# Optimization experiments

Measured on AMD Instinct MI355X. Metric: run time of the kernel, lower is better.

## Reference

```python
import jax, jax.numpy as jnp
import numpy as np

B, S, H = 2, 2048, 2048
NH, HD = 32, 64          # num heads, head dim (H = NH*HD)
ROT = 16                 # rotary_ndims = int(HD * rope_pct=0.25)
THETA = 10000.0
MAXPOS = 4096
NEG_INF = -1e30


def _rope_cache():
    inv_freq = 1.0 / (THETA ** (jnp.arange(0, ROT, 2, dtype=jnp.float32) / ROT))
    t = jnp.arange(MAXPOS, dtype=jnp.float32)
    freqs = jnp.outer(t, inv_freq)              # [MAXPOS, ROT/2]
    emb = jnp.concatenate([freqs, freqs], -1)   # [MAXPOS, ROT]
    return jnp.cos(emb), jnp.sin(emb)


def _rotate_half(x):
    x1, x2 = jnp.split(x, 2, axis=-1)
    return jnp.concatenate([-x2, x1], axis=-1)


def setup_inputs() -> dict:
    key = jax.random.key(0)
    k1, k2, k3 = jax.random.split(key, 3)
    hidden_states = jax.random.normal(k1, (B, S, H), dtype=jnp.float32)
    qkv_w = jax.random.normal(k2, (3 * H, H), dtype=jnp.float32) * 0.02
    o_w = jax.random.normal(k3, (H, H), dtype=jnp.float32) * 0.02
    position_ids = (jnp.arange(B * S).reshape(B, S) % MAXPOS).astype(jnp.int32)
    return {"hidden_states": hidden_states, "qkv_w": qkv_w, "o_w": o_w,
            "position_ids": position_ids}


def reference(hidden_states, qkv_w, o_w, position_ids):
    b, s, _ = hidden_states.shape
    # fused QKV projection (Linear, no bias): x @ W^T
    qkv = hidden_states @ qkv_w.T                      # [b, s, 3H]
    q, k, v = jnp.split(qkv, 3, axis=-1)
    # (b, s, nh*hd) -> (b, nh, s, hd)
    q = q.reshape(b, s, NH, HD).transpose(0, 2, 1, 3)
    k = k.reshape(b, s, NH, HD).transpose(0, 2, 1, 3)
    v = v.reshape(b, s, NH, HD).transpose(0, 2, 1, 3)

    # partial RoPE on first ROT dims
    cos, sin = _rope_cache()
    cos = cos[position_ids][:, None]                   # [b, 1, s, ROT]
    sin = sin[position_ids][:, None]
    q_rot, q_pass = q[..., :ROT], q[..., ROT:]
    k_rot, k_pass = k[..., :ROT], k[..., ROT:]
    q_rot = q_rot * cos + _rotate_half(q_rot) * sin
    k_rot = k_rot * cos + _rotate_half(k_rot) * sin
    q = jnp.concatenate([q_rot, q_pass], axis=-1)
    k = jnp.concatenate([k_rot, k_pass], axis=-1)

    # causal scaled-dot-product attention (prefill branch, layer_past=None)
    scale = 1.0 / jnp.sqrt(jnp.float32(HD))
    scores = jnp.einsum('bhqd,bhkd->bhqk', q, k) * scale
    causal = jnp.tril(jnp.ones((s, s), dtype=bool))
    scores = jnp.where(causal, scores, NEG_INF)
    weights = jax.nn.softmax(scores.astype(jnp.float32), axis=-1).astype(q.dtype)
    attn = jnp.einsum('bhqk,bhkd->bhqd', weights, v)   # [b, nh, s, hd]

    attn = attn.transpose(0, 2, 1, 3).reshape(b, s, NH * HD)
    return attn @ o_w.T
```

## Files before the change

kernel.cpp:

```cpp
#include <hip/hip_runtime.h>
#include <hip/hip_bf16.h>
#include <math.h>

#define B_   2
#define S_   2048
#define H_   2048
#define NH_  32
#define HD_  64

typedef __bf16 bf16_t;
typedef bf16_t bf16x8 __attribute__((ext_vector_type(8)));
typedef float  f32x4  __attribute__((ext_vector_type(4)));

__device__ __forceinline__ float bf2f(unsigned short u) {
  unsigned int x = ((unsigned int)u) << 16;
  return __builtin_bit_cast(float, x);
}
__device__ __forceinline__ unsigned short f2bf(float f) {
  unsigned int u = __builtin_bit_cast(unsigned int, f);
  u += 0x7FFFu + ((u >> 16) & 1u);
  return (unsigned short)(u >> 16);
}

__device__ __forceinline__ void gload16(const void* g, void* l) {
  __builtin_amdgcn_global_load_lds((const __attribute__((address_space(1))) void*)g,
                                   (__attribute__((address_space(3))) void*)l, 16, 0, 0);
}

__global__ void cast_kernel(const float* __restrict__ in, unsigned short* __restrict__ out, int n4) {
  int stride = gridDim.x * blockDim.x;
  for (int i = blockIdx.x * blockDim.x + threadIdx.x; i < n4; i += stride) {
    float4 v = reinterpret_cast<const float4*>(in)[i];
    ushort4 o;
    o.x = f2bf(v.x); o.y = f2bf(v.y); o.z = f2bf(v.z); o.w = f2bf(v.w);
    reinterpret_cast<ushort4*>(out)[i] = o;
  }
}

template<int EPI>
__global__ __launch_bounds__(256) void gemm_bt(
    const unsigned short* __restrict__ A, const unsigned short* __restrict__ Bt,
    float* __restrict__ outF,
    unsigned short* __restrict__ qb, unsigned short* __restrict__ kb, unsigned short* __restrict__ vt,
    int M, int N, int K)
{
  __shared__ unsigned short As[128 * 64];
  __shared__ unsigned short Bs[128 * 64];
  const int tid  = threadIdx.x;
  const int lane = tid & 63;
  const int wave = tid >> 6;
  const int lo = lane & 15, hi = lane >> 4;
  const int wr = wave >> 1, wc = wave & 1;
  const int m0 = blockIdx.x * 128;
  const int n0 = blockIdx.y * 128;

  const unsigned short* asrc[4];
  const unsigned short* bsrc[4];
  unsigned short* adst[4];
  unsigned short* bdst[4];
#pragma unroll
  for (int i = 0; i < 4; ++i) {
    int idx = i * 256 + tid;
    int r  = idx >> 3;
    int cb = (idx & 7) * 16;
    int cs = cb ^ ((r & 7) << 4);
    asrc[i] = A  + (size_t)(m0 + r) * K + (cs >> 1);
    bsrc[i] = Bt + (size_t)(n0 + r) * K + (cs >> 1);
    adst[i] = &As[idx * 8];
    bdst[i] = &Bs[idx * 8];
  }

  f32x4 zero = {0.f, 0.f, 0.f, 0.f};
  f32x4 acc[4][4];
#pragma unroll
  for (int i = 0; i < 4; ++i)
#pragma unroll
    for (int j = 0; j < 4; ++j) acc[i][j] = zero;

  for (int k0 = 0; k0 < K; k0 += 64) {
    __syncthreads();
#pragma unroll
    for (int i = 0; i < 4; ++i) gload16(asrc[i] + k0, adst[i]);
#pragma unroll
    for (int i = 0; i < 4; ++i) gload16(bsrc[i] + k0, bdst[i]);
    __syncthreads();
#pragma unroll
    for (int kk = 0; kk < 2; ++kk) {
      bf16x8 af[4], bfm[4];
#pragma unroll
      for (int i = 0; i < 4; ++i) {
        int ra = wr * 64 + i * 16 + lo;
        af[i] = *reinterpret_cast<const bf16x8*>(
            (const char*)As + ra * 128 + ((kk * 64 + hi * 16) ^ ((ra & 7) << 4)));
        int rb = wc * 64 + i * 16 + lo;
        bfm[i] = *reinterpret_cast<const bf16x8*>(
            (const char*)Bs + rb * 128 + ((kk * 64 + hi * 16) ^ ((rb & 7) << 4)));
      }
#pragma unroll
      for (int i = 0; i < 4; ++i)
#pragma unroll
        for (int j = 0; j < 4; ++j)
          acc[i][j] = __builtin_amdgcn_mfma_f32_16x16x32_bf16(af[i], bfm[j], acc[i][j], 0, 0, 0);
    }
  }

#pragma unroll
  for (int i = 0; i < 4; ++i) {
#pragma unroll
    for (int j = 0; j < 4; ++j) {
#pragma unroll
      for (int r = 0; r < 4; ++r) {
        int row = m0 + wr * 64 + i * 16 + hi * 4 + r;
        int col = n0 + wc * 64 + j * 16 + lo;
        float v = acc[i][j][r];
        if (EPI == 0) {
          int sec = col >> 11;
          int hh  = (col >> 6) & 31;
          int d   = col & 63;
          int b   = row >> 11;
          int s   = row & 2047;
          unsigned short bv = f2bf(v);
          if (sec == 0)      qb[((size_t)(b * NH_ + hh) * S_ + s) * HD_ + d] = bv;
          else if (sec == 1) kb[((size_t)(b * NH_ + hh) * S_ + s) * HD_ + d] = bv;
          else               vt[((size_t)(b * NH_ + hh) * HD_ + d) * S_ + s] = bv;
        } else {
          outF[(size_t)row * N + col] = v;
        }
      }
    }
  }
}

__global__ void rope_kernel(unsigned short* __restrict__ qb, unsigned short* __restrict__ kb,
                            const int* __restrict__ pos) {
  int idx = blockIdx.x * blockDim.x + threadIdx.x;
  if (idx >= B_ * NH_ * S_) return;
  int s  = idx & (S_ - 1);
  int bh = idx >> 11;
  int b  = bh >> 5;
  float p = (float)pos[b * S_ + s];
  const float invf[8] = {1.0f, 0.31622776601683794f, 0.1f, 0.031622776601683791f,
                         0.01f, 0.0031622776601683794f, 0.001f, 0.00031622776601683794f};
  unsigned short* q = qb + (size_t)idx * HD_;
  unsigned short* k = kb + (size_t)idx * HD_;
#pragma unroll
  for (int i = 0; i < 8; ++i) {
    float ang = p * invf[i];
    float sn, c;
    sincosf(ang, &sn, &c);
    float q1 = bf2f(q[i]), q2 = bf2f(q[i + 8]);
    q[i]     = f2bf(q1 * c - q2 * sn);
    q[i + 8] = f2bf(q2 * c + q1 * sn);
    float k1 = bf2f(k[i]), k2 = bf2f(k[i + 8]);
    k[i]     = f2bf(k1 * c - k2 * sn);
    k[i + 8] = f2bf(k2 * c + k1 * sn);
  }
}

__global__ __launch_bounds__(256) void attn_fwd(
    const unsigned short* __restrict__ qb, const unsigned short* __restrict__ kb,
    const unsigned short* __restrict__ vt, unsigned short* __restrict__ ob)
{
  __shared__ unsigned short Ks[2][64 * 64];
  __shared__ unsigned short Vs[2][64 * 64];
  __shared__ unsigned short Ps[4][32 * 64];
  const int qt   = (int)gridDim.x - 1 - (int)blockIdx.x;
  const int bh   = blockIdx.y;
  const int tid  = threadIdx.x;
  const int lane = tid & 63;
  const int wave = tid >> 6;
  const int lo = lane & 15, hi = lane >> 4;
  const int b = bh >> 5, h = bh & 31;
  const unsigned short* Qg = qb + (size_t)bh * S_ * HD_;
  const unsigned short* Kg = kb + (size_t)bh * S_ * HD_;
  const unsigned short* Vg = vt + (size_t)bh * HD_ * S_;

  bf16x8 aq[2][2];
#pragma unroll
  for (int rf = 0; rf < 2; ++rf)
#pragma unroll
    for (int kk = 0; kk < 2; ++kk) {
      bf16x8 t = *reinterpret_cast<const bf16x8*>(
          Qg + (size_t)(qt * 128 + wave * 32 + rf * 16 + lo) * HD_ + kk * 32 + hi * 8);
#pragma unroll
      for (int e = 0; e < 8; ++e) aq[rf][kk][e] = (bf16_t)((float)t[e] * 0.125f);
    }

  f32x4 zero = {0.f, 0.f, 0.f, 0.f};
  float m_s[2][4], l_s[2][4];
  f32x4 o_acc[2][4];
#pragma unroll
  for (int rf = 0; rf < 2; ++rf)
#pragma unroll
    for (int r = 0; r < 4; ++r) { m_s[rf][r] = -1e30f; l_s[rf][r] = 0.f; }
#pragma unroll
  for (int rf = 0; rf < 2; ++rf)
#pragma unroll
    for (int dt = 0; dt < 4; ++dt) o_acc[rf][dt] = zero;

  auto stage = [&](int kt, int buf) {
#pragma unroll
    for (int i = 0; i < 2; ++i) {
      int idx = i * 256 + tid;
      int r   = idx >> 3;
      int cs  = ((idx & 7) * 16) ^ ((r & 7) << 4);
      gload16(Kg + (size_t)(kt * 64 + r) * HD_ + (cs >> 1), &Ks[buf][idx * 8]);
      gload16(Vg + (size_t)r * S_ + kt * 64 + (cs >> 1), &Vs[buf][idx * 8]);
    }
  };

  const int nkt = 2 * qt + 2;
  stage(0, 0);

  for (int kt = 0; kt < nkt; ++kt) {
    const int cur = kt & 1;
    if (kt + 1 < nkt) {
      stage(kt + 1, cur ^ 1);
      asm volatile("s_waitcnt vmcnt(4)" ::: "memory");
    } else {
      asm volatile("s_waitcnt vmcnt(0)" ::: "memory");
    }
    __builtin_amdgcn_s_barrier();
    __builtin_amdgcn_sched_barrier(0);

    bf16x8 bk[4][2];
#pragma unroll
    for (int ct = 0; ct < 4; ++ct)
#pragma unroll
      for (int kk = 0; kk < 2; ++kk) {
        int row = ct * 16 + lo;
        bk[ct][kk] = *reinterpret_cast<const bf16x8*>(
            (const char*)&Ks[cur][0] + row * 128 + ((kk * 64 + hi * 16) ^ ((row & 7) << 4)));
      }
    f32x4 sc[2][4];
    __builtin_amdgcn_s_setprio(1);
#pragma unroll
    for (int rf = 0; rf < 2; ++rf)
#pragma unroll
      for (int ct = 0; ct < 4; ++ct) {
        f32x4 a = zero;
        a = __builtin_amdgcn_mfma_f32_16x16x32_bf16(aq[rf][0], bk[ct][0], a, 0, 0, 0);
        a = __builtin_amdgcn_mfma_f32_16x16x32_bf16(aq[rf][1], bk[ct][1], a, 0, 0, 0);
        sc[rf][ct] = a;
      }
    __builtin_amdgcn_s_setprio(0);

    if (kt >= nkt - 2) {
#pragma unroll
      for (int rf = 0; rf < 2; ++rf)
#pragma unroll
        for (int ct = 0; ct < 4; ++ct)
#pragma unroll
          for (int rr = 0; rr < 4; ++rr) {
            int qrow = qt * 128 + wave * 32 + rf * 16 + hi * 4 + rr;
            int kcol = kt * 64 + ct * 16 + lo;
            if (kcol > qrow) sc[rf][ct][rr] = -1e30f;
          }
    }

#pragma unroll
    for (int rf = 0; rf < 2; ++rf) {
#pragma unroll
      for (int rr = 0; rr < 4; ++rr) {
        float tm = fmaxf(fmaxf(sc[rf][0][rr], sc[rf][1][rr]),
                         fmaxf(sc[rf][2][rr], sc[rf][3][rr]));
        tm = fmaxf(tm, __shfl_xor(tm, 1));
        tm = fmaxf(tm, __shfl_xor(tm, 2));
        tm = fmaxf(tm, __shfl_xor(tm, 4));
        tm = fmaxf(tm, __shfl_xor(tm, 8));
        float mn = fmaxf(m_s[rf][rr], tm);
        float corr = __expf(m_s[rf][rr] - mn);
        m_s[rf][rr] = mn;
        float rs = 0.f;
#pragma unroll
        for (int ct = 0; ct < 4; ++ct) {
          float e = __expf(sc[rf][ct][rr] - mn);
          sc[rf][ct][rr] = e;
          rs += e;
        }
        rs += __shfl_xor(rs, 1);
        rs += __shfl_xor(rs, 2);
        rs += __shfl_xor(rs, 4);
        rs += __shfl_xor(rs, 8);
        l_s[rf][rr] = l_s[rf][rr] * corr + rs;
#pragma unroll
        for (int dt = 0; dt < 4; ++dt) o_acc[rf][dt][rr] *= corr;
      }
    }

    char* pw = (char*)&Ps[wave][0];
#pragma unroll
    for (int rf = 0; rf < 2; ++rf)
#pragma unroll
      for (int ct = 0; ct < 4; ++ct)
#pragma unroll
        for (int rr = 0; rr < 4; ++rr) {
          int row = rf * 16 + hi * 4 + rr;
          *(unsigned short*)(pw + row * 128 + ((2 * (ct * 16 + lo)) ^ ((row & 7) << 4))) =
              f2bf(sc[rf][ct][rr]);
        }
    bf16x8 ap[2][2];
#pragma unroll
    for (int rf = 0; rf < 2; ++rf)
#pragma unroll
      for (int kk = 0; kk < 2; ++kk) {
        int rowA = rf * 16 + lo;
        ap[rf][kk] = *reinterpret_cast<const bf16x8*>(
            pw + rowA * 128 + ((kk * 64 + hi * 16) ^ ((rowA & 7) << 4)));
      }

    bf16x8 bv[4][2];
#pragma unroll
    for (int dt = 0; dt < 4; ++dt)
#pragma unroll
      for (int kk = 0; kk < 2; ++kk) {
        int row = dt * 16 + lo;
        bv[dt][kk] = *reinterpret_cast<const bf16x8*>(
            (const char*)&Vs[cur][0] + row * 128 + ((kk * 64 + hi * 16) ^ ((row & 7) << 4)));
      }
    __builtin_amdgcn_s_setprio(1);
#pragma unroll
    for (int rf = 0; rf < 2; ++rf)
#pragma unroll
      for (int dt = 0; dt < 4; ++dt) {
        o_acc[rf][dt] = __builtin_amdgcn_mfma_f32_16x16x32_bf16(ap[rf][0], bv[dt][0], o_acc[rf][dt], 0, 0, 0);
        o_acc[rf][dt] = __builtin_amdgcn_mfma_f32_16x16x32_bf16(ap[rf][1], bv[dt][1], o_acc[rf][dt], 0, 0, 0);
      }
    __builtin_amdgcn_s_setprio(0);

    __builtin_amdgcn_s_barrier();
    __builtin_amdgcn_sched_barrier(0);
  }

#pragma unroll
  for (int rf = 0; rf < 2; ++rf) {
    float inv_l[4];
#pragma unroll
    for (int rr = 0; rr < 4; ++rr) inv_l[rr] = 1.f / l_s[rf][rr];
#pragma unroll
    for (int dt = 0; dt < 4; ++dt)
#pragma unroll
      for (int rr = 0; rr < 4; ++rr) {
        int srow = qt * 128 + wave * 32 + rf * 16 + hi * 4 + rr;
        int d    = dt * 16 + lo;
        ob[(size_t)(b * S_ + srow) * H_ + h * HD_ + d] = f2bf(o_acc[rf][dt][rr] * inv_l[rr]);
      }
  }
}

extern "C" void kernel_launch(void* const* d_in, const int* in_sizes, int n_in,
                              void* d_out, int out_size, void* d_ws, size_t ws_size,
                              hipStream_t stream) {
  (void)in_sizes; (void)n_in; (void)out_size; (void)ws_size;
  const float* hs   = (const float*)d_in[0];
  const float* qkvw = (const float*)d_in[1];
  const float* ow   = (const float*)d_in[2];
  const int*   pos  = (const int*)d_in[3];

  char* ws = (char*)d_ws;
  unsigned short* Xb = (unsigned short*)(ws);
  unsigned short* Wq = (unsigned short*)(ws + (16ull << 20));
  unsigned short* Ob = (unsigned short*)(ws + (40ull << 20));
  unsigned short* Qb = (unsigned short*)(ws + (48ull << 20));
  unsigned short* Kb = (unsigned short*)(ws + (64ull << 20));
  unsigned short* Vt = (unsigned short*)(ws + (80ull << 20));

  cast_kernel<<<2048, 256, 0, stream>>>(hs,   Xb, (B_ * S_ * H_) / 4);
  cast_kernel<<<2048, 256, 0, stream>>>(qkvw, Wq, (3 * H_ * H_) / 4);
  cast_kernel<<<2048, 256, 0, stream>>>(ow,   Ob, (H_ * H_) / 4);

  gemm_bt<0><<<dim3(32, 48), 256, 0, stream>>>(Xb, Wq, nullptr, Qb, Kb, Vt,
                                               B_ * S_, 3 * H_, H_);
  rope_kernel<<<(B_ * NH_ * S_) / 256, 256, 0, stream>>>(Qb, Kb, pos);
  attn_fwd<<<dim3(S_ / 128, B_ * NH_), 256, 0, stream>>>(Qb, Kb, Vt, Xb);
  gemm_bt<1><<<dim3(32, 16), 256, 0, stream>>>(Xb, Ob, (float*)d_out,
                                               nullptr, nullptr, nullptr,
                                               B_ * S_, H_, H_);
}
```

Measured before the change: 572.8 us.

## Widen attention blocks to 256 query rows with triple-buffered KV and causal skip

The attention kernel now uses 512-thread blocks covering 256 query rows, so each staged K/V tile is shared by twice as many waves. K/V staging moves to a 3-deep ring buffer that prefetches two tiles ahead. Waves skip compute on tiles lying wholly above their causal diagonal, and the softmax uses exp2 with log2e folded into the Q scale. In exchange, work per block becomes less balanced across waves, LDS use grows, and the launch-bounds hint may restrict registers.

```diff
diff --git a/kernel.cpp b/kernel.cpp
--- a/kernel.cpp
+++ b/kernel.cpp
@@ -157,13 +157,13 @@
   }
 }
 
-__global__ __launch_bounds__(256) void attn_fwd(
+__global__ __launch_bounds__(512, 3) void attn_fwd(
     const unsigned short* __restrict__ qb, const unsigned short* __restrict__ kb,
     const unsigned short* __restrict__ vt, unsigned short* __restrict__ ob)
 {
-  __shared__ unsigned short Ks[2][64 * 64];
-  __shared__ unsigned short Vs[2][64 * 64];
-  __shared__ unsigned short Ps[4][32 * 64];
+  __shared__ unsigned short Ks[3][64 * 64];
+  __shared__ unsigned short Vs[3][64 * 64];
+  __shared__ unsigned short Ps[8][32 * 64];
   const int qt   = (int)gridDim.x - 1 - (int)blockIdx.x;
   const int bh   = blockIdx.y;
   const int tid  = threadIdx.x;
@@ -175,15 +175,18 @@
   const unsigned short* Kg = kb + (size_t)bh * S_ * HD_;
   const unsigned short* Vg = vt + (size_t)bh * HD_ * S_;
 
+  const int qrow0 = qt * 256 + wave * 32;
+
+  const float qscale = 0.125f * 1.4426950408889634f;
   bf16x8 aq[2][2];
 #pragma unroll
   for (int rf = 0; rf < 2; ++rf)
 #pragma unroll
     for (int kk = 0; kk < 2; ++kk) {
       bf16x8 t = *reinterpret_cast<const bf16x8*>(
-          Qg + (size_t)(qt * 128 + wave * 32 + rf * 16 + lo) * HD_ + kk * 32 + hi * 8);
-#pragma unroll
-      for (int e = 0; e < 8; ++e) aq[rf][kk][e] = (bf16_t)((float)t[e] * 0.125f);
+          Qg + (size_t)(qrow0 + rf * 16 + lo) * HD_ + kk * 32 + hi * 8);
+#pragma unroll
+      for (int e = 0; e < 8; ++e) aq[rf][kk][e] = (bf16_t)((float)t[e] * qscale);
     }
 
   f32x4 zero = {0.f, 0.f, 0.f, 0.f};
@@ -199,134 +202,135 @@
     for (int dt = 0; dt < 4; ++dt) o_acc[rf][dt] = zero;
 
   auto stage = [&](int kt, int buf) {
-#pragma unroll
-    for (int i = 0; i < 2; ++i) {
-      int idx = i * 256 + tid;
-      int r   = idx >> 3;
-      int cs  = ((idx & 7) * 16) ^ ((r & 7) << 4);
-      gload16(Kg + (size_t)(kt * 64 + r) * HD_ + (cs >> 1), &Ks[buf][idx * 8]);
-      gload16(Vg + (size_t)r * S_ + kt * 64 + (cs >> 1), &Vs[buf][idx * 8]);
-    }
+    int r  = tid >> 3;
+    int cs = ((tid & 7) * 16) ^ ((r & 7) << 4);
+    gload16(Kg + (size_t)(kt * 64 + r) * HD_ + (cs >> 1), &Ks[buf][tid * 8]);
+    gload16(Vg + (size_t)r * S_ + kt * 64 + (cs >> 1), &Vs[buf][tid * 8]);
   };
 
-  const int nkt = 2 * qt + 2;
+  const int nkt = 4 * qt + 4;
   stage(0, 0);
+  stage(1, 1);
 
   for (int kt = 0; kt < nkt; ++kt) {
-    const int cur = kt & 1;
-    if (kt + 1 < nkt) {
-      stage(kt + 1, cur ^ 1);
+    const int cur = kt % 3;
+    if (kt + 2 < nkt) {
+      stage(kt + 2, (kt + 2) % 3);
       asm volatile("s_waitcnt vmcnt(4)" ::: "memory");
+    } else if (kt + 2 == nkt) {
+      asm volatile("s_waitcnt vmcnt(2)" ::: "memory");
     } else {
       asm volatile("s_waitcnt vmcnt(0)" ::: "memory");
     }
     __builtin_amdgcn_s_barrier();
     __builtin_amdgcn_sched_barrier(0);
 
-    bf16x8 bk[4][2];
-#pragma unroll
-    for (int ct = 0; ct < 4; ++ct)
-#pragma unroll
-      for (int kk = 0; kk < 2; ++kk) {
-        int row = ct * 16 + lo;
-        bk[ct][kk] = *reinterpret_cast<const bf16x8*>(
-            (const char*)&Ks[cur][0] + row * 128 + ((kk * 64 + hi * 16) ^ ((row & 7) << 4)));
-      }
-    f32x4 sc[2][4];
-    __builtin_amdgcn_s_setprio(1);
-#pragma unroll
-    for (int rf = 0; rf < 2; ++rf)
-#pragma unroll
-      for (int ct = 0; ct < 4; ++ct) {
-        f32x4 a = zero;
-        a = __builtin_amdgcn_mfma_f32_16x16x32_bf16(aq[rf][0], bk[ct][0], a, 0, 0, 0);
-        a = __builtin_amdgcn_mfma_f32_16x16x32_bf16(aq[rf][1], bk[ct][1], a, 0, 0, 0);
-        sc[rf][ct] = a;
-      }
-    __builtin_amdgcn_s_setprio(0);
-
-    if (kt >= nkt - 2) {
+    if (kt * 64 <= qrow0 + 31) {
+      bf16x8 bk[4][2];
+#pragma unroll
+      for (int ct = 0; ct < 4; ++ct)
+#pragma unroll
+        for (int kk = 0; kk < 2; ++kk) {
+          int row = ct * 16 + lo;
+          bk[ct][kk] = *reinterpret_cast<const bf16x8*>(
+              (const char*)&Ks[cur][0] + row * 128 + ((kk * 64 + hi * 16) ^ ((row & 7) << 4)));
+        }
+      f32x4 sc[2][4];
+      __builtin_amdgcn_s_setprio(1);
 #pragma unroll
       for (int rf = 0; rf < 2; ++rf)
 #pragma unroll
+        for (int ct = 0; ct < 4; ++ct) {
+          f32x4 a = zero;
+          a = __builtin_amdgcn_mfma_f32_16x16x32_bf16(aq[rf][0], bk[ct][0], a, 0, 0, 0);
+          a = __builtin_amdgcn_mfma_f32_16x16x32_bf16(aq[rf][1], bk[ct][1], a, 0, 0, 0);
+          sc[rf][ct] = a;
+        }
+      __builtin_amdgcn_s_setprio(0);
+
+      if (kt * 64 + 63 > qrow0) {
+#pragma unroll
+        for (int rf = 0; rf < 2; ++rf)
+#pragma unroll
+          for (int ct = 0; ct < 4; ++ct)
+#pragma unroll
+            for (int rr = 0; rr < 4; ++rr) {
+              int qrow = qrow0 + rf * 16 + hi * 4 + rr;
+              int kcol = kt * 64 + ct * 16 + lo;
+              if (kcol > qrow) sc[rf][ct][rr] = -1e30f;
+            }
+      }
+
+#pragma unroll
+      for (int rf = 0; rf < 2; ++rf) {
+#pragma unroll
+        for (int rr = 0; rr < 4; ++rr) {
+          float tm = fmaxf(fmaxf(sc[rf][0][rr], sc[rf][1][rr]),
+                           fmaxf(sc[rf][2][rr], sc[rf][3][rr]));
+          tm = fmaxf(tm, __shfl_xor(tm, 1));
+          tm = fmaxf(tm, __shfl_xor(tm, 2));
+          tm = fmaxf(tm, __shfl_xor(tm, 4));
+          tm = fmaxf(tm, __shfl_xor(tm, 8));
+          float mn = fmaxf(m_s[rf][rr], tm);
+          float corr = exp2f(m_s[rf][rr] - mn);
+          m_s[rf][rr] = mn;
+          float rs = 0.f;
+#pragma unroll
+          for (int ct = 0; ct < 4; ++ct) {
+            float e = exp2f(sc[rf][ct][rr] - mn);
+            sc[rf][ct][rr] = e;
+            rs += e;
+          }
+          rs += __shfl_xor(rs, 1);
+          rs += __shfl_xor(rs, 2);
+          rs += __shfl_xor(rs, 4);
+          rs += __shfl_xor(rs, 8);
+          l_s[rf][rr] = l_s[rf][rr] * corr + rs;
+#pragma unroll
+          for (int dt = 0; dt < 4; ++dt) o_acc[rf][dt][rr] *= corr;
+        }
+      }
+
+      char* pw = (char*)&Ps[wave][0];
+#pragma unroll
+      for (int rf = 0; rf < 2; ++rf)
+#pragma unroll
         for (int ct = 0; ct < 4; ++ct)
 #pragma unroll
           for (int rr = 0; rr < 4; ++rr) {
-            int qrow = qt * 128 + wave * 32 + rf * 16 + hi * 4 + rr;
-            int kcol = kt * 64 + ct * 16 + lo;
-            if (kcol > qrow) sc[rf][ct][rr] = -1e30f;
+            int row = rf * 16 + hi * 4 + rr;
+            *(unsigned short*)(pw + row * 128 + ((2 * (ct * 16 + lo)) ^ ((row & 7) << 4))) =
+                f2bf(sc[rf][ct][rr]);
           }
-    }
-
-#pragma unroll
-    for (int rf = 0; rf < 2; ++rf) {
-#pragma unroll
-      for (int rr = 0; rr < 4; ++rr) {
-        float tm = fmaxf(fmaxf(sc[rf][0][rr], sc[rf][1][rr]),
-                         fmaxf(sc[rf][2][rr], sc[rf][3][rr]));
-        tm = fmaxf(tm, __shfl_xor(tm, 1));
-        tm = fmaxf(tm, __shfl_xor(tm, 2));
-        tm = fmaxf(tm, __shfl_xor(tm, 4));
-        tm = fmaxf(tm, __shfl_xor(tm, 8));
-        float mn = fmaxf(m_s[rf][rr], tm);
-        float corr = __expf(m_s[rf][rr] - mn);
-        m_s[rf][rr] = mn;
-        float rs = 0.f;
-#pragma unroll
-        for (int ct = 0; ct < 4; ++ct) {
-          float e = __expf(sc[rf][ct][rr] - mn);
-          sc[rf][ct][rr] = e;
-          rs += e;
-        }
-        rs += __shfl_xor(rs, 1);
-        rs += __shfl_xor(rs, 2);
-        rs += __shfl_xor(rs, 4);
-        rs += __shfl_xor(rs, 8);
-        l_s[rf][rr] = l_s[rf][rr] * corr + rs;
-#pragma unroll
-        for (int dt = 0; dt < 4; ++dt) o_acc[rf][dt][rr] *= corr;
-      }
-    }
-
-    char* pw = (char*)&Ps[wave][0];
-#pragma unroll
-    for (int rf = 0; rf < 2; ++rf)
-#pragma unroll
-      for (int ct = 0; ct < 4; ++ct)
-#pragma unroll
-        for (int rr = 0; rr < 4; ++rr) {
-          int row = rf * 16 + hi * 4 + rr;
-          *(unsigned short*)(pw + row * 128 + ((2 * (ct * 16 + lo)) ^ ((row & 7) << 4))) =
-              f2bf(sc[rf][ct][rr]);
-        }
-    bf16x8 ap[2][2];
-#pragma unroll
-    for (int rf = 0; rf < 2; ++rf)
-#pragma unroll
-      for (int kk = 0; kk < 2; ++kk) {
-        int rowA = rf * 16 + lo;
-        ap[rf][kk] = *reinterpret_cast<const bf16x8*>(
-            pw + rowA * 128 + ((kk * 64 + hi * 16) ^ ((rowA & 7) << 4)));
-      }
-
-    bf16x8 bv[4][2];
-#pragma unroll
-    for (int dt = 0; dt < 4; ++dt)
-#pragma unroll
-      for (int kk = 0; kk < 2; ++kk) {
-        int row = dt * 16 + lo;
-        bv[dt][kk] = *reinterpret_cast<const bf16x8*>(
-            (const char*)&Vs[cur][0] + row * 128 + ((kk * 64 + hi * 16) ^ ((row & 7) << 4)));
-      }
-    __builtin_amdgcn_s_setprio(1);
-#pragma unroll
-    for (int rf = 0; rf < 2; ++rf)
-#pragma unroll
-      for (int dt = 0; dt < 4; ++dt) {
-        o_acc[rf][dt] = __builtin_amdgcn_mfma_f32_16x16x32_bf16(ap[rf][0], bv[dt][0], o_acc[rf][dt], 0, 0, 0);
-        o_acc[rf][dt] = __builtin_amdgcn_mfma_f32_16x16x32_bf16(ap[rf][1], bv[dt][1], o_acc[rf][dt], 0, 0, 0);
-      }
-    __builtin_amdgcn_s_setprio(0);
+      bf16x8 ap[2][2];
+#pragma unroll
+      for (int rf = 0; rf < 2; ++rf)
+#pragma unroll
+        for (int kk = 0; kk < 2; ++kk) {
+          int rowA = rf * 16 + lo;
+          ap[rf][kk] = *reinterpret_cast<const bf16x8*>(
+              pw + rowA * 128 + ((kk * 64 + hi * 16) ^ ((rowA & 7) << 4)));
+        }
+
+      bf16x8 bv[4][2];
+#pragma unroll
+      for (int dt = 0; dt < 4; ++dt)
+#pragma unroll
+        for (int kk = 0; kk < 2; ++kk) {
+          int row = dt * 16 + lo;
+          bv[dt][kk] = *reinterpret_cast<const bf16x8*>(
+              (const char*)&Vs[cur][0] + row * 128 + ((kk * 64 + hi * 16) ^ ((row & 7) << 4)));
+        }
+      __builtin_amdgcn_s_setprio(1);
+#pragma unroll
+      for (int rf = 0; rf < 2; ++rf)
+#pragma unroll
+        for (int dt = 0; dt < 4; ++dt) {
+          o_acc[rf][dt] = __builtin_amdgcn_mfma_f32_16x16x32_bf16(ap[rf][0], bv[dt][0], o_acc[rf][dt], 0, 0, 0);
+          o_acc[rf][dt] = __builtin_amdgcn_mfma_f32_16x16x32_bf16(ap[rf][1], bv[dt][1], o_acc[rf][dt], 0, 0, 0);
+        }
+      __builtin_amdgcn_s_setprio(0);
+    }
 
     __builtin_amdgcn_s_barrier();
     __builtin_amdgcn_sched_barrier(0);
@@ -341,7 +345,7 @@
     for (int dt = 0; dt < 4; ++dt)
 #pragma unroll
       for (int rr = 0; rr < 4; ++rr) {
-        int srow = qt * 128 + wave * 32 + rf * 16 + hi * 4 + rr;
+        int srow = qrow0 + rf * 16 + hi * 4 + rr;
         int d    = dt * 16 + lo;
         ob[(size_t)(b * S_ + srow) * H_ + h * HD_ + d] = f2bf(o_acc[rf][dt][rr] * inv_l[rr]);
       }
@@ -372,7 +376,7 @@
   gemm_bt<0><<<dim3(32, 48), 256, 0, stream>>>(Xb, Wq, nullptr, Qb, Kb, Vt,
                                                B_ * S_, 3 * H_, H_);
   rope_kernel<<<(B_ * NH_ * S_) / 256, 256, 0, stream>>>(Qb, Kb, pos);
-  attn_fwd<<<dim3(S_ / 128, B_ * NH_), 256, 0, stream>>>(Qb, Kb, Vt, Xb);
+  attn_fwd<<<dim3(S_ / 256, B_ * NH_), 512, 0, stream>>>(Qb, Kb, Vt, Xb);
   gemm_bt<1><<<dim3(32, 16), 256, 0, stream>>>(Xb, Ob, (float*)d_out,
                                                nullptr, nullptr, nullptr,
                                                B_ * S_, H_, H_);
```

New measurement: 597.2 us. 4.3% more time.

## Pair causal query tiles per block to balance attention work and share K/V loads

Applied to the files above, without the earlier changes.

Each attention block now processes two query tiles, j and 15-j, so every block does the same amount of causal work, and the K/V tiles it stages are shared by both. The grid drops from 1024 to 512 blocks with a flat index, and launch bounds now request two blocks per CU. The softmax switches to exp2f with log2(e) folded into the Q scale. The cost is doubled accumulator and register state per wave and a larger P scratch buffer in LDS, which may limit occupancy.

```diff
diff --git a/kernel.cpp b/kernel.cpp
--- a/kernel.cpp
+++ b/kernel.cpp
@@ -157,15 +157,16 @@
   }
 }
 
-__global__ __launch_bounds__(256) void attn_fwd(
+__global__ __launch_bounds__(256, 2) void attn_fwd(
     const unsigned short* __restrict__ qb, const unsigned short* __restrict__ kb,
     const unsigned short* __restrict__ vt, unsigned short* __restrict__ ob)
 {
   __shared__ unsigned short Ks[2][64 * 64];
   __shared__ unsigned short Vs[2][64 * 64];
-  __shared__ unsigned short Ps[4][32 * 64];
-  const int qt   = (int)gridDim.x - 1 - (int)blockIdx.x;
-  const int bh   = blockIdx.y;
+  __shared__ unsigned short Ps[4][2][32 * 64];
+  const int bid  = blockIdx.x;
+  const int j    = bid >> 6;
+  const int bh   = bid & 63;
   const int tid  = threadIdx.x;
   const int lane = tid & 63;
   const int wave = tid >> 6;
@@ -175,28 +176,35 @@
   const unsigned short* Kg = kb + (size_t)bh * S_ * HD_;
   const unsigned short* Vg = vt + (size_t)bh * HD_ * S_;
 
-  bf16x8 aq[2][2];
-#pragma unroll
-  for (int rf = 0; rf < 2; ++rf)
-#pragma unroll
-    for (int kk = 0; kk < 2; ++kk) {
-      bf16x8 t = *reinterpret_cast<const bf16x8*>(
-          Qg + (size_t)(qt * 128 + wave * 32 + rf * 16 + lo) * HD_ + kk * 32 + hi * 8);
-#pragma unroll
-      for (int e = 0; e < 8; ++e) aq[rf][kk][e] = (bf16_t)((float)t[e] * 0.125f);
-    }
+  const int qt[2]    = {j, 15 - j};
+  const int qrow0[2] = {j * 128 + wave * 32, (15 - j) * 128 + wave * 32};
+
+  const float qscale = 0.125f * 1.4426950408889634f;
+  bf16x8 aq[2][2][2];
+#pragma unroll
+  for (int t = 0; t < 2; ++t)
+#pragma unroll
+    for (int rf = 0; rf < 2; ++rf)
+#pragma unroll
+      for (int kk = 0; kk < 2; ++kk) {
+        bf16x8 tt = *reinterpret_cast<const bf16x8*>(
+            Qg + (size_t)(qrow0[t] + rf * 16 + lo) * HD_ + kk * 32 + hi * 8);
+#pragma unroll
+        for (int e = 0; e < 8; ++e) aq[t][rf][kk][e] = (bf16_t)((float)tt[e] * qscale);
+      }
 
   f32x4 zero = {0.f, 0.f, 0.f, 0.f};
-  float m_s[2][4], l_s[2][4];
-  f32x4 o_acc[2][4];
-#pragma unroll
-  for (int rf = 0; rf < 2; ++rf)
-#pragma unroll
-    for (int r = 0; r < 4; ++r) { m_s[rf][r] = -1e30f; l_s[rf][r] = 0.f; }
-#pragma unroll
-  for (int rf = 0; rf < 2; ++rf)
-#pragma unroll
-    for (int dt = 0; dt < 4; ++dt) o_acc[rf][dt] = zero;
+  float m_s[2][2][4], l_s[2][2][4];
+  f32x4 o_acc[2][2][4];
+#pragma unroll
+  for (int t = 0; t < 2; ++t)
+#pragma unroll
+    for (int rf = 0; rf < 2; ++rf)
+#pragma unroll
+      for (int r = 0; r < 4; ++r) {
+        m_s[t][rf][r] = -1e30f; l_s[t][rf][r] = 0.f;
+        o_acc[t][rf][r] = zero;
+      }
 
   auto stage = [&](int kt, int buf) {
 #pragma unroll
@@ -209,7 +217,7 @@
     }
   };
 
-  const int nkt = 2 * qt + 2;
+  const int nkt = 2 * (15 - j) + 2;
   stage(0, 0);
 
   for (int kt = 0; kt < nkt; ++kt) {
@@ -232,82 +240,79 @@
         bk[ct][kk] = *reinterpret_cast<const bf16x8*>(
             (const char*)&Ks[cur][0] + row * 128 + ((kk * 64 + hi * 16) ^ ((row & 7) << 4)));
       }
-    f32x4 sc[2][4];
-    __builtin_amdgcn_s_setprio(1);
-#pragma unroll
-    for (int rf = 0; rf < 2; ++rf)
-#pragma unroll
-      for (int ct = 0; ct < 4; ++ct) {
-        f32x4 a = zero;
-        a = __builtin_amdgcn_mfma_f32_16x16x32_bf16(aq[rf][0], bk[ct][0], a, 0, 0, 0);
-        a = __builtin_amdgcn_mfma_f32_16x16x32_bf16(aq[rf][1], bk[ct][1], a, 0, 0, 0);
-        sc[rf][ct] = a;
-      }
-    __builtin_amdgcn_s_setprio(0);
-
-    if (kt >= nkt - 2) {
-#pragma unroll
-      for (int rf = 0; rf < 2; ++rf)
-#pragma unroll
-        for (int ct = 0; ct < 4; ++ct)
+
+#pragma unroll
+    for (int t = 0; t < 2; ++t) {
+      if (kt * 64 <= qrow0[t] + 31) {
+        f32x4 sc[2][4];
+        __builtin_amdgcn_s_setprio(1);
+#pragma unroll
+        for (int rf = 0; rf < 2; ++rf)
+#pragma unroll
+          for (int ct = 0; ct < 4; ++ct) {
+            f32x4 a = zero;
+            a = __builtin_amdgcn_mfma_f32_16x16x32_bf16(aq[t][rf][0], bk[ct][0], a, 0, 0, 0);
+            a = __builtin_amdgcn_mfma_f32_16x16x32_bf16(aq[t][rf][1], bk[ct][1], a, 0, 0, 0);
+            sc[rf][ct] = a;
+          }
+        __builtin_amdgcn_s_setprio(0);
+
+        if (kt * 64 + 63 > qrow0[t]) {
+#pragma unroll
+          for (int rf = 0; rf < 2; ++rf)
+#pragma unroll
+            for (int ct = 0; ct < 4; ++ct)
+#pragma unroll
+              for (int rr = 0; rr < 4; ++rr) {
+                int qrow = qrow0[t] + rf * 16 + hi * 4 + rr;
+                int kcol = kt * 64 + ct * 16 + lo;
+                if (kcol > qrow) sc[rf][ct][rr] = -1e30f;
+              }
+        }
+
+#pragma unroll
+        for (int rf = 0; rf < 2; ++rf) {
 #pragma unroll
           for (int rr = 0; rr < 4; ++rr) {
-            int qrow = qt * 128 + wave * 32 + rf * 16 + hi * 4 + rr;
-            int kcol = kt * 64 + ct * 16 + lo;
-            if (kcol > qrow) sc[rf][ct][rr] = -1e30f;
+            float tm = fmaxf(fmaxf(sc[rf][0][rr], sc[rf][1][rr]),
+                             fmaxf(sc[rf][2][rr], sc[rf][3][rr]));
+            tm = fmaxf(tm, __shfl_xor(tm, 1));
+            tm = fmaxf(tm, __shfl_xor(tm, 2));
+            tm = fmaxf(tm, __shfl_xor(tm, 4));
+            tm = fmaxf(tm, __shfl_xor(tm, 8));
+            float mn = fmaxf(m_s[t][rf][rr], tm);
+            float corr = exp2f(m_s[t][rf][rr] - mn);
+            m_s[t][rf][rr] = mn;
+            float rs = 0.f;
+#pragma unroll
+            for (int ct = 0; ct < 4; ++ct) {
+              float e = exp2f(sc[rf][ct][rr] - mn);
+              sc[rf][ct][rr] = e;
+              rs += e;
+            }
+            rs += __shfl_xor(rs, 1);
+            rs += __shfl_xor(rs, 2);
+            rs += __shfl_xor(rs, 4);
+            rs += __shfl_xor(rs, 8);
+            l_s[t][rf][rr] = l_s[t][rf][rr] * corr + rs;
+#pragma unroll
+            for (int dt = 0; dt < 4; ++dt) o_acc[t][rf][dt][rr] *= corr;
           }
-    }
-
-#pragma unroll
-    for (int rf = 0; rf < 2; ++rf) {
-#pragma unroll
-      for (int rr = 0; rr < 4; ++rr) {
-        float tm = fmaxf(fmaxf(sc[rf][0][rr], sc[rf][1][rr]),
-                         fmaxf(sc[rf][2][rr], sc[rf][3][rr]));
-        tm = fmaxf(tm, __shfl_xor(tm, 1));
-        tm = fmaxf(tm, __shfl_xor(tm, 2));
-        tm = fmaxf(tm, __shfl_xor(tm, 4));
-        tm = fmaxf(tm, __shfl_xor(tm, 8));
-        float mn = fmaxf(m_s[rf][rr], tm);
-        float corr = __expf(m_s[rf][rr] - mn);
-        m_s[rf][rr] = mn;
-        float rs = 0.f;
-#pragma unroll
-        for (int ct = 0; ct < 4; ++ct) {
-          float e = __expf(sc[rf][ct][rr] - mn);
-          sc[rf][ct][rr] = e;
-          rs += e;
         }
-        rs += __shfl_xor(rs, 1);
-        rs += __shfl_xor(rs, 2);
-        rs += __shfl_xor(rs, 4);
-        rs += __shfl_xor(rs, 8);
-        l_s[rf][rr] = l_s[rf][rr] * corr + rs;
-#pragma unroll
-        for (int dt = 0; dt < 4; ++dt) o_acc[rf][dt][rr] *= corr;
-      }
-    }
-
-    char* pw = (char*)&Ps[wave][0];
-#pragma unroll
-    for (int rf = 0; rf < 2; ++rf)
-#pragma unroll
-      for (int ct = 0; ct < 4; ++ct)
-#pragma unroll
-        for (int rr = 0; rr < 4; ++rr) {
-          int row = rf * 16 + hi * 4 + rr;
-          *(unsigned short*)(pw + row * 128 + ((2 * (ct * 16 + lo)) ^ ((row & 7) << 4))) =
-              f2bf(sc[rf][ct][rr]);
-        }
-    bf16x8 ap[2][2];
-#pragma unroll
-    for (int rf = 0; rf < 2; ++rf)
-#pragma unroll
-      for (int kk = 0; kk < 2; ++kk) {
-        int rowA = rf * 16 + lo;
-        ap[rf][kk] = *reinterpret_cast<const bf16x8*>(
-            pw + rowA * 128 + ((kk * 64 + hi * 16) ^ ((rowA & 7) << 4)));
-      }
+
+        char* pw = (char*)&Ps[wave][t][0];
+#pragma unroll
+        for (int rf = 0; rf < 2; ++rf)
+#pragma unroll
+          for (int ct = 0; ct < 4; ++ct)
+#pragma unroll
+            for (int rr = 0; rr < 4; ++rr) {
+              int row = rf * 16 + hi * 4 + rr;
+              *(unsigned short*)(pw + row * 128 + ((2 * (ct * 16 + lo)) ^ ((row & 7) << 4))) =
+                  f2bf(sc[rf][ct][rr]);
+            }
+      }
+    }
 
     bf16x8 bv[4][2];
 #pragma unroll
@@ -318,34 +323,51 @@
         bv[dt][kk] = *reinterpret_cast<const bf16x8*>(
             (const char*)&Vs[cur][0] + row * 128 + ((kk * 64 + hi * 16) ^ ((row & 7) << 4)));
       }
-    __builtin_amdgcn_s_setprio(1);
-#pragma unroll
-    for (int rf = 0; rf < 2; ++rf)
-#pragma unroll
-      for (int dt = 0; dt < 4; ++dt) {
-        o_acc[rf][dt] = __builtin_amdgcn_mfma_f32_16x16x32_bf16(ap[rf][0], bv[dt][0], o_acc[rf][dt], 0, 0, 0);
-        o_acc[rf][dt] = __builtin_amdgcn_mfma_f32_16x16x32_bf16(ap[rf][1], bv[dt][1], o_acc[rf][dt], 0, 0, 0);
-      }
-    __builtin_amdgcn_s_setprio(0);
+#pragma unroll
+    for (int t = 0; t < 2; ++t) {
+      if (kt * 64 <= qrow0[t] + 31) {
+        char* pw = (char*)&Ps[wave][t][0];
+        bf16x8 ap[2][2];
+#pragma unroll
+        for (int rf = 0; rf < 2; ++rf)
+#pragma unroll
+          for (int kk = 0; kk < 2; ++kk) {
+            int rowA = rf * 16 + lo;
+            ap[rf][kk] = *reinterpret_cast<const bf16x8*>(
+                pw + rowA * 128 + ((kk * 64 + hi * 16) ^ ((rowA & 7) << 4)));
+          }
+        __builtin_amdgcn_s_setprio(1);
+#pragma unroll
+        for (int rf = 0; rf < 2; ++rf)
+#pragma unroll
+          for (int dt = 0; dt < 4; ++dt) {
+            o_acc[t][rf][dt] = __builtin_amdgcn_mfma_f32_16x16x32_bf16(ap[rf][0], bv[dt][0], o_acc[t][rf][dt], 0, 0, 0);
+            o_acc[t][rf][dt] = __builtin_amdgcn_mfma_f32_16x16x32_bf16(ap[rf][1], bv[dt][1], o_acc[t][rf][dt], 0, 0, 0);
+          }
+        __builtin_amdgcn_s_setprio(0);
+      }
+    }
 
     __builtin_amdgcn_s_barrier();
     __builtin_amdgcn_sched_barrier(0);
   }
 
 #pragma unroll
-  for (int rf = 0; rf < 2; ++rf) {
-    float inv_l[4];
-#pragma unroll
-    for (int rr = 0; rr < 4; ++rr) inv_l[rr] = 1.f / l_s[rf][rr];
-#pragma unroll
-    for (int dt = 0; dt < 4; ++dt)
-#pragma unroll
-      for (int rr = 0; rr < 4; ++rr) {
-        int srow = qt * 128 + wave * 32 + rf * 16 + hi * 4 + rr;
-        int d    = dt * 16 + lo;
-        ob[(size_t)(b * S_ + srow) * H_ + h * HD_ + d] = f2bf(o_acc[rf][dt][rr] * inv_l[rr]);
-      }
-  }
+  for (int t = 0; t < 2; ++t)
+#pragma unroll
+    for (int rf = 0; rf < 2; ++rf) {
+      float inv_l[4];
+#pragma unroll
+      for (int rr = 0; rr < 4; ++rr) inv_l[rr] = 1.f / l_s[t][rf][rr];
+#pragma unroll
+      for (int dt = 0; dt < 4; ++dt)
+#pragma unroll
+        for (int rr = 0; rr < 4; ++rr) {
+          int srow = qrow0[t] + rf * 16 + hi * 4 + rr;
+          int d    = dt * 16 + lo;
+          ob[(size_t)(b * S_ + srow) * H_ + h * HD_ + d] = f2bf(o_acc[t][rf][dt][rr] * inv_l[rr]);
+        }
+    }
 }
 
 extern "C" void kernel_launch(void* const* d_in, const int* in_sizes, int n_in,
@@ -372,7 +394,7 @@
   gemm_bt<0><<<dim3(32, 48), 256, 0, stream>>>(Xb, Wq, nullptr, Qb, Kb, Vt,
                                                B_ * S_, 3 * H_, H_);
   rope_kernel<<<(B_ * NH_ * S_) / 256, 256, 0, stream>>>(Qb, Kb, pos);
-  attn_fwd<<<dim3(S_ / 128, B_ * NH_), 256, 0, stream>>>(Qb, Kb, Vt, Xb);
+  attn_fwd<<<512, 256, 0, stream>>>(Qb, Kb, Vt, Xb);
   gemm_bt<1><<<dim3(32, 16), 256, 0, stream>>>(Xb, Ob, (float*)d_out,
                                                nullptr, nullptr, nullptr,
                                                B_ * S_, H_, H_);
```

Result: faster. 499.7 us (-12.8%).
